# Optimization experiments

Hardware: AMD Instinct MI355X
Metric: run time of the kernel (lower is better)

Reference implementation:

```python
import jax, jax.numpy as jnp
import numpy as np

N = 16384      # nodes
E = 262144     # edges (avg degree 16)
R = 9          # relation types
D_IN = 384     # embed_size
D_H = 768      # hidden_size
N_CLASSES = 5


def setup_inputs() -> dict:
    key = jax.random.key(0)
    ks = jax.random.split(key, 11)
    s = 0.02
    return {
        "x": jax.random.normal(ks[0], (N, D_IN), jnp.float32),
        "edge_index": jax.random.randint(ks[1], (2, E), 0, N, dtype=jnp.int64)
        if jax.config.jax_enable_x64 else jax.random.randint(ks[1], (2, E), 0, N).astype(jnp.int32),
        "edge_type": jax.random.randint(ks[2], (E,), 0, R).astype(jnp.int32),
        "rel_W": jax.random.normal(ks[3], (R, D_H, D_IN), jnp.float32) * s,
        "rel_b": jax.random.normal(ks[4], (R, D_H), jnp.float32) * s,
        "norm_constants": jnp.ones((R,), jnp.float32),
        "mp_lin_W": jax.random.normal(ks[5], (D_H, D_H), jnp.float32) * s,
        "mp_lin_b": jax.random.normal(ks[6], (D_H,), jnp.float32) * s,
        "mp_self_W": jax.random.normal(ks[7], (D_H, D_H), jnp.float32) * s,
        "mp_self_b": jax.random.normal(ks[8], (D_H,), jnp.float32) * s,
        "out_W": jax.random.normal(ks[9], (N_CLASSES, D_H), jnp.float32) * s,
        "out_b": jax.random.normal(ks[10], (N_CLASSES,), jnp.float32) * s,
    }


def reference(x, edge_index, edge_type, rel_W, rel_b, norm_constants,
              mp_lin_W, mp_lin_b, mp_self_W, mp_self_b, out_W, out_b):
    n = x.shape[0]
    src = edge_index[0]  # j : message source (x_j)
    dst = edge_index[1]  # i : aggregation target

    # --- RelationAwareMP ---
    # edge_weights[i, j] from x @ x.T, computed per edge (identical math)
    ew = jnp.einsum('ed,ed->e', x[dst], x[src])                  # [E]
    norm = ew / norm_constants[edge_type]                        # [E]
    # per-relation linear applied to all nodes, then gathered per edge
    h = jnp.einsum('nd,rhd->rnh', x, rel_W) + rel_b[:, None, :]  # [R,N,H]
    msg = h[edge_type, src]                                      # [E,H]
    aggr = jax.ops.segment_sum(norm[:, None] * msg, dst, num_segments=n)
    x1 = jax.nn.relu(aggr)                                       # [N,H]

    # --- MP (add aggregation + self transform) ---
    self_x = x1 @ mp_self_W.T + mp_self_b
    hm = x1 @ mp_lin_W.T + mp_lin_b
    aggr2 = jax.ops.segment_sum(hm[src], dst, num_segments=n)
    x2 = jax.nn.relu(aggr2 + self_x)                             # [N,H]

    # --- readout ---
    pooled = x2.mean(axis=0)                                     # [H]
    return pooled @ out_W.T + out_b                              # [N_CLASSES]
```

## Files before the change

kernel.cpp:

```cpp
#include <hip/hip_runtime.h>

typedef unsigned char  u8;
typedef unsigned short u16;
typedef unsigned int   u32;

#define NN   16384
#define EE   262144
#define RR   9
#define DIN  384
#define DH   768
#define KSU  3456
#define KS   3488

typedef float  f32x4 __attribute__((ext_vector_type(4)));
typedef float  f32x2 __attribute__((ext_vector_type(2)));
typedef __bf16 b16x8 __attribute__((ext_vector_type(8)));

__device__ __forceinline__ u16 f2bf(float f){
  u32 u = __builtin_bit_cast(u32, f);
  u += 0x7fffu + ((u >> 16) & 1u);
  return (u16)(u >> 16);
}
__device__ __forceinline__ float bf2f(u16 h){
  u32 u = ((u32)h) << 16;
  return __builtin_bit_cast(float, u);
}
__device__ __forceinline__ float bflo(u32 u){ return __builtin_bit_cast(float, u << 16); }
__device__ __forceinline__ float bfhi(u32 u){ return __builtin_bit_cast(float, u & 0xffff0000u); }
__device__ __forceinline__ u32 pk2(float a, float b){
  return (u32)f2bf(a) | ((u32)f2bf(b) << 16);
}
__device__ __forceinline__ void gll16(const void* g, void* l){
  __builtin_amdgcn_global_load_lds((const __attribute__((address_space(1))) void*)g,
                                   (__attribute__((address_space(3))) void*)l, 16, 0, 0);
}

__global__ void k_count(const int* __restrict__ dst, int* __restrict__ counts){
  const int e = blockIdx.x*256 + threadIdx.x;
  if (e < EE) atomicAdd(&counts[dst[e]], 1);
}

__global__ __launch_bounds__(1024) void k_scan(const int* __restrict__ counts,
                                               int* __restrict__ starts,
                                               int* __restrict__ cursor){
  __shared__ int tot[1024];
  const int t = threadIdx.x;
  int loc[16]; int s = 0;
  #pragma unroll
  for (int j=0;j<16;j++){ loc[j] = counts[t*16+j]; s += loc[j]; }
  tot[t] = s;
  __syncthreads();
  for (int o=1;o<1024;o<<=1){
    int v = (t>=o) ? tot[t-o] : 0;
    __syncthreads();
    tot[t] += v;
    __syncthreads();
  }
  int run = tot[t] - s;
  #pragma unroll
  for (int j=0;j<16;j++){ starts[t*16+j] = run; cursor[t*16+j] = run; run += loc[j]; }
  if (t == 1023) starts[NN] = run;
}

__global__ void k_place(const int* __restrict__ src, const int* __restrict__ dst,
                        const int* __restrict__ et, int* __restrict__ cursor,
                        int* __restrict__ srcp, int* __restrict__ dstp,
                        int* __restrict__ rp){
  const int e = blockIdx.x*256 + threadIdx.x;
  if (e < EE){
    const int p = atomicAdd(&cursor[dst[e]], 1);
    srcp[p] = src[e];
    dstp[p] = dst[e];
    rp[p]   = et[e];
  }
}

#define NXP (NN*DIN/2)
#define NW1 (DH*KS)
#define NW2 (2*DH*DH)
__global__ __launch_bounds__(256) void k_conv(const float* __restrict__ x,
                                              const float* __restrict__ rW,
                                              const float* __restrict__ rb,
                                              const float* __restrict__ lW,
                                              const float* __restrict__ sW,
                                              u32* __restrict__ xb,
                                              u16* __restrict__ Wst,
                                              u16* __restrict__ WB){
  long j = (long)blockIdx.x*256 + threadIdx.x;
  if (j < NXP){
    const f32x2 v = ((const f32x2*)x)[j];
    xb[j] = pk2(v.x, v.y);
    return;
  }
  j -= NXP;
  if (j < NW1){
    const int hh = (int)(j / KS);
    const int k  = (int)(j - (long)hh*KS);
    float v;
    if (k < KSU){ const int r = k / DIN; const int d = k - r*DIN;
                  v = rW[((long)r*DH + hh)*DIN + d]; }
    else if (k < KSU + RR){ const int r = k - KSU; v = rb[(long)r*DH + hh]; }
    else v = 0.f;
    Wst[(long)hh*KS + k] = f2bf(v);
    return;
  }
  j -= NW1;
  const float v = (j < DH*DH) ? lW[j] : sW[j - DH*DH];
  WB[j] = f2bf(v);
}

__global__ __launch_bounds__(256, 4) void k_dots(const u32* __restrict__ xb,
                                                 const int* __restrict__ srcp,
                                                 const int* __restrict__ dstp,
                                                 const int* __restrict__ rp,
                                                 const float* __restrict__ nc,
                                                 float* __restrict__ normp){
  const int p = blockIdx.x*4 + (threadIdx.x >> 6);
  const int l = threadIdx.x & 63;
  const u32* xs = xb + (long)srcp[p]*192;
  const u32* xd = xb + (long)dstp[p]*192;
  float s = 0.f;
  #pragma unroll
  for (int j=0;j<3;j++){
    const u32 a = xs[l + 64*j], b = xd[l + 64*j];
    s += bflo(a)*bflo(b) + bfhi(a)*bfhi(b);
  }
  #pragma unroll
  for (int o=32;o;o>>=1) s += __shfl_xor(s, o);
  if (l == 0) normp[p] = s / nc[rp[p]];
}

__global__ __launch_bounds__(256, 3) void k_phase1f(const u32* __restrict__ xb,
                                                    const int* __restrict__ srcp,
                                                    const int* __restrict__ rp,
                                                    const float* __restrict__ normp,
                                                    const int* __restrict__ starts,
                                                    u16* __restrict__ s){
  const int w = threadIdx.x >> 6, l = threadIdx.x & 63;
  const int i = blockIdx.x*4 + w;
  float acc[RR][6];
  float cacc[RR];
  #pragma unroll
  for (int r=0;r<RR;r++){
    cacc[r] = 0.f;
    #pragma unroll
    for (int j=0;j<6;j++) acc[r][j] = 0.f;
  }
  const int e0 = starts[i], np = starts[i+1] - e0;

  u32 A0=0,A1=0,A2=0,B0=0,B1=0,B2=0,C0=0,C1=0,C2=0;
  float nA=0.f,nB=0.f,nC=0.f; int Ar=0,Br=0,Cr=0;

  #define LOADSLOT(S0,S1,S2,NR,RV,idx) { \
    const u32* xs_ = xb + (long)srcp[idx]*192; \
    S0 = xs_[l]; S1 = xs_[64+l]; S2 = xs_[128+l]; \
    NR = normp[idx]; RV = rp[idx]; }
  #define CONSUME(S0,S1,S2,NR,RV) { \
    const float f0=bflo(S0), f1=bfhi(S0), f2=bflo(S1), \
                f3=bfhi(S1), f4=bflo(S2), f5=bfhi(S2); \
    const float nm = NR; \
    switch (RV){ \
      case 0: cacc[0]+=nm; acc[0][0]+=nm*f0; acc[0][1]+=nm*f1; acc[0][2]+=nm*f2; acc[0][3]+=nm*f3; acc[0][4]+=nm*f4; acc[0][5]+=nm*f5; break; \
      case 1: cacc[1]+=nm; acc[1][0]+=nm*f0; acc[1][1]+=nm*f1; acc[1][2]+=nm*f2; acc[1][3]+=nm*f3; acc[1][4]+=nm*f4; acc[1][5]+=nm*f5; break; \
      case 2: cacc[2]+=nm; acc[2][0]+=nm*f0; acc[2][1]+=nm*f1; acc[2][2]+=nm*f2; acc[2][3]+=nm*f3; acc[2][4]+=nm*f4; acc[2][5]+=nm*f5; break; \
      case 3: cacc[3]+=nm; acc[3][0]+=nm*f0; acc[3][1]+=nm*f1; acc[3][2]+=nm*f2; acc[3][3]+=nm*f3; acc[3][4]+=nm*f4; acc[3][5]+=nm*f5; break; \
      case 4: cacc[4]+=nm; acc[4][0]+=nm*f0; acc[4][1]+=nm*f1; acc[4][2]+=nm*f2; acc[4][3]+=nm*f3; acc[4][4]+=nm*f4; acc[4][5]+=nm*f5; break; \
      case 5: cacc[5]+=nm; acc[5][0]+=nm*f0; acc[5][1]+=nm*f1; acc[5][2]+=nm*f2; acc[5][3]+=nm*f3; acc[5][4]+=nm*f4; acc[5][5]+=nm*f5; break; \
      case 6: cacc[6]+=nm; acc[6][0]+=nm*f0; acc[6][1]+=nm*f1; acc[6][2]+=nm*f2; acc[6][3]+=nm*f3; acc[6][4]+=nm*f4; acc[6][5]+=nm*f5; break; \
      case 7: cacc[7]+=nm; acc[7][0]+=nm*f0; acc[7][1]+=nm*f1; acc[7][2]+=nm*f2; acc[7][3]+=nm*f3; acc[7][4]+=nm*f4; acc[7][5]+=nm*f5; break; \
      default:cacc[8]+=nm; acc[8][0]+=nm*f0; acc[8][1]+=nm*f1; acc[8][2]+=nm*f2; acc[8][3]+=nm*f3; acc[8][4]+=nm*f4; acc[8][5]+=nm*f5; break; \
    } }

  if (np > 0) LOADSLOT(A0,A1,A2,nA,Ar,e0)
  if (np > 1) LOADSLOT(B0,B1,B2,nB,Br,e0+1)
  if (np > 2) LOADSLOT(C0,C1,C2,nC,Cr,e0+2)

  for (int p=0; p<np; p+=3){
    CONSUME(A0,A1,A2,nA,Ar)
    if (p+3 < np) LOADSLOT(A0,A1,A2,nA,Ar,e0+p+3)
    if (p+1 < np){
      CONSUME(B0,B1,B2,nB,Br)
      if (p+4 < np) LOADSLOT(B0,B1,B2,nB,Br,e0+p+4)
    }
    if (p+2 < np){
      CONSUME(C0,C1,C2,nC,Cr)
      if (p+5 < np) LOADSLOT(C0,C1,C2,nC,Cr,e0+p+5)
    }
  }
  #undef CONSUME
  #undef LOADSLOT

  u16* srow = s + (long)i*KS;
  #pragma unroll
  for (int r=0;r<RR;r++){
    #pragma unroll
    for (int seg=0;seg<3;seg++)
      ((u32*)(srow + r*DIN + seg*128))[l] = pk2(acc[r][seg*2], acc[r][seg*2+1]);
  }
  float cv = 0.f;
  #pragma unroll
  for (int r=0;r<RR;r++) cv = (l == r) ? cacc[r] : cv;
  if (l < 32) srow[KSU + l] = f2bf(l < RR ? cv : 0.f);
}

template<int MODE>
__global__ __launch_bounds__(256, 2)
void k_gemm_bt(const u16* __restrict__ A, const u16* __restrict__ B,
               int M, int N, int K,
               u16* __restrict__ O0, u16* __restrict__ O1,
               const float* __restrict__ b0, const float* __restrict__ b1)
{
  __shared__ __align__(16) u16 As[128*32];
  __shared__ __align__(16) u16 Bs[128*32];
  const int t  = threadIdx.x;
  const int wv = t >> 6;
  const int ln = t & 63;
  const int wm = wv >> 1, wn = wv & 1;
  const long m0 = (long)blockIdx.x * 128;
  const long n0 = (long)blockIdx.y * 128;

  const int ri    = ln >> 2;
  const int kw    = (ri + (ri >> 2)) & 3;
  const int skcol = (((ln & 3) - kw) & 3) * 8;

  f32x4 acc[4][4];
  #pragma unroll
  for (int i=0;i<4;i++)
    #pragma unroll
    for (int j=0;j<4;j++) acc[i][j] = {0.f,0.f,0.f,0.f};

  const int fr = ln & 15, fq = ln >> 4;
  const int kr    = (fr + (fr >> 2)) & 3;
  const int rdoff = ((fq + kr) & 3) * 8;
  const int nk = K >> 5;
  for (int kb=0; kb<nk; ++kb){
    const long k0 = (long)kb * 32;
    #pragma unroll
    for (int q=0;q<2;q++){
      const int seg = wv*2 + q;
      const int row = seg*16 + ri;
      gll16(A + (m0 + row)*(long)K + k0 + skcol, &As[seg*512]);
      gll16(B + (n0 + row)*(long)K + k0 + skcol, &Bs[seg*512]);
    }
    __syncthreads();
    b16x8 av[4], bv[4];
    #pragma unroll
    for (int i=0;i<4;i++){
      av[i] = *(const b16x8*)&As[(wm*64 + i*16 + fr)*32 + rdoff];
      bv[i] = *(const b16x8*)&Bs[(wn*64 + i*16 + fr)*32 + rdoff];
    }
    #pragma unroll
    for (int i=0;i<4;i++)
      #pragma unroll
      for (int j=0;j<4;j++)
        acc[i][j] = __builtin_amdgcn_mfma_f32_16x16x32_bf16(av[i], bv[j], acc[i][j], 0, 0, 0);
    __syncthreads();
  }

  #pragma unroll
  for (int i=0;i<4;i++){
    #pragma unroll
    for (int j=0;j<4;j++){
      #pragma unroll
      for (int r=0;r<4;r++){
        const long m = m0 + wm*64 + i*16 + fq*4 + r;
        const long n = n0 + wn*64 + j*16 + fr;
        float v = acc[i][j][r];
        if (MODE == 0){
          v = v > 0.f ? v : 0.f;
          O0[m*DH + n] = f2bf(v);
        } else {
          if (n < DH) O0[m*DH + n]      = f2bf(v + b0[n]);
          else        O1[m*DH + (n-DH)] = f2bf(v + b1[n-DH]);
        }
      }
    }
  }
}

__global__ __launch_bounds__(256, 4) void k_phase2(const u32* __restrict__ hm32,
                                                   const u32* __restrict__ sfx32,
                                                   const int* __restrict__ srcp,
                                                   const int* __restrict__ starts,
                                                   float* __restrict__ pooled8){
  const int w = threadIdx.x >> 6, l = threadIdx.x & 63;
  const int t = threadIdx.x;
  __shared__ float pl[DH];
  #pragma unroll
  for (int k=0;k<3;k++) pl[t + 256*k] = 0.f;
  __syncthreads();

  float po[12];
  #pragma unroll
  for (int j=0;j<12;j++) po[j] = 0.f;

  for (int q=0;q<2;q++){
    const int i = blockIdx.x*8 + w*2 + q;
    float a[12];
    #pragma unroll
    for (int j=0;j<12;j++) a[j] = 0.f;
    const int e0 = starts[i], np = starts[i+1] - e0;

    u32 A0=0,A1=0,A2=0,A3=0,A4=0,A5=0;
    u32 B0=0,B1=0,B2=0,B3=0,B4=0,B5=0;
    if (np > 0){
      const u32* hr = hm32 + (long)srcp[e0]*384;
      A0=hr[l]; A1=hr[64+l]; A2=hr[128+l]; A3=hr[192+l]; A4=hr[256+l]; A5=hr[320+l];
    }
    if (np > 1){
      const u32* hr = hm32 + (long)srcp[e0+1]*384;
      B0=hr[l]; B1=hr[64+l]; B2=hr[128+l]; B3=hr[192+l]; B4=hr[256+l]; B5=hr[320+l];
    }
    for (int p=0; p<np; p+=2){
      a[0]+=bflo(A0); a[1]+=bfhi(A0); a[2]+=bflo(A1); a[3] +=bfhi(A1);
      a[4]+=bflo(A2); a[5]+=bfhi(A2); a[6] +=bflo(A3); a[7] +=bfhi(A3);
      a[8]+=bflo(A4); a[9]+=bfhi(A4); a[10]+=bflo(A5); a[11]+=bfhi(A5);
      if (p+2 < np){
        const u32* hr = hm32 + (long)srcp[e0+p+2]*384;
        A0=hr[l]; A1=hr[64+l]; A2=hr[128+l]; A3=hr[192+l]; A4=hr[256+l]; A5=hr[320+l];
      }
      if (p+1 < np){
        a[0]+=bflo(B0); a[1]+=bfhi(B0); a[2] +=bflo(B1); a[3] +=bfhi(B1);
        a[4]+=bflo(B2); a[5]+=bfhi(B2); a[6] +=bflo(B3); a[7] +=bfhi(B3);
        a[8]+=bflo(B4); a[9]+=bfhi(B4); a[10]+=bflo(B5); a[11]+=bfhi(B5);
        if (p+3 < np){
          const u32* hr = hm32 + (long)srcp[e0+p+3]*384;
          B0=hr[l]; B1=hr[64+l]; B2=hr[128+l]; B3=hr[192+l]; B4=hr[256+l]; B5=hr[320+l];
        }
      }
    }
    const u32* sr = sfx32 + (long)i*384;
    #pragma unroll
    for (int j=0;j<6;j++){
      const u32 sv = sr[l + 64*j];
      float v0 = a[2*j]   + bflo(sv);
      float v1 = a[2*j+1] + bfhi(sv);
      po[2*j]   += v0 > 0.f ? v0 : 0.f;
      po[2*j+1] += v1 > 0.f ? v1 : 0.f;
    }
  }
  #pragma unroll
  for (int j=0;j<6;j++){
    atomicAdd(&pl[2*l   + 128*j], po[2*j]);
    atomicAdd(&pl[2*l+1 + 128*j], po[2*j+1]);
  }
  __syncthreads();
  float* pd = pooled8 + (blockIdx.x & 7)*DH;
  #pragma unroll
  for (int k=0;k<3;k++) atomicAdd(&pd[t + 256*k], pl[t + 256*k]);
}

__global__ __launch_bounds__(256) void k_final(const float* __restrict__ pooled8,
                                               const float* __restrict__ oW,
                                               const float* __restrict__ ob,
                                               float* __restrict__ out){
  __shared__ float ps[DH];
  __shared__ float red[256];
  const int t = threadIdx.x;
  for (int h=t; h<DH; h+=256){
    float s = 0.f;
    #pragma unroll
    for (int c=0;c<8;c++) s += pooled8[c*DH + h];
    ps[h] = s;
  }
  __syncthreads();
  for (int c=0;c<5;c++){
    float p = 0.f;
    for (int h=t; h<DH; h+=256) p += ps[h]*oW[c*DH + h];
    red[t] = p; __syncthreads();
    for (int o=128;o;o>>=1){ if (t<o) red[t]+=red[t+o]; __syncthreads(); }
    if (t == 0) out[c] = red[0]*(1.f/(float)NN) + ob[c];
    __syncthreads();
  }
}

extern "C" void kernel_launch(void* const* d_in, const int* in_sizes, int n_in,
                              void* d_out, int out_size, void* d_ws, size_t ws_size,
                              hipStream_t stream)
{
  (void)in_sizes; (void)n_in; (void)out_size; (void)ws_size;
  const float* x     = (const float*)d_in[0];
  const int*   ei    = (const int*)  d_in[1];
  const int*   et    = (const int*)  d_in[2];
  const float* relW  = (const float*)d_in[3];
  const float* relb  = (const float*)d_in[4];
  const float* nc    = (const float*)d_in[5];
  const float* linW  = (const float*)d_in[6];
  const float* linb  = (const float*)d_in[7];
  const float* selfW = (const float*)d_in[8];
  const float* selfb = (const float*)d_in[9];
  const float* outW  = (const float*)d_in[10];
  const float* outb  = (const float*)d_in[11];
  float* out = (float*)d_out;

  u8* w = (u8*)d_ws;
  int*   counts  = (int*)(w + 0);
  int*   starts  = (int*)(w + 65536);
  int*   cursor  = (int*)(w + 131328);
  int*   srcp    = (int*)(w + 196864);
  int*   dstp    = (int*)(w + 1245440);
  int*   rp      = (int*)(w + 2294016);
  float* normp   = (float*)(w + 3342592);
  u16*   Wst     = (u16*)(w + 4391168);
  u16*   WB      = (u16*)(w + 9748736);
  u16*   x1      = (u16*)(w + 12108032);
  u32*   xb      = (u32*)x1;
  float* pooled8 = (float*)(w + 37273856);
  u16*   S       = (u16*)(w + 37298432);
  u16*   hm      = S;
  u16*   sfx     = (u16*)(w + 37298432 + 25165824);

  const int* esrc = ei;
  const int* edst = ei + EE;

  hipMemsetAsync(counts, 0, NN*sizeof(int), stream);
  hipMemsetAsync(pooled8, 0, 8*DH*sizeof(float), stream);

  k_count <<<EE/256, 256, 0, stream>>>(edst, counts);
  k_scan  <<<1, 1024, 0, stream>>>(counts, starts, cursor);
  k_place <<<EE/256, 256, 0, stream>>>(esrc, edst, et, cursor, srcp, dstp, rp);
  k_conv  <<<(NXP + NW1 + NW2)/256, 256, 0, stream>>>(x, relW, relb, linW, selfW,
                                                      xb, Wst, WB);
  k_dots  <<<EE/4, 256, 0, stream>>>(xb, srcp, dstp, rp, nc, normp);
  k_phase1f<<<NN/4, 256, 0, stream>>>(xb, srcp, rp, normp, starts, S);
  k_gemm_bt<0><<<dim3(NN/128, DH/128), 256, 0, stream>>>(
      S, Wst, NN, DH, KS, x1, (u16*)nullptr, (const float*)nullptr, (const float*)nullptr);
  k_gemm_bt<1><<<dim3(NN/128, 2*DH/128), 256, 0, stream>>>(
      x1, WB, NN, 2*DH, DH, hm, sfx, linb, selfb);
  k_phase2<<<NN/8, 256, 0, stream>>>((const u32*)hm, (const u32*)sfx, srcp, starts, pooled8);
  k_final <<<1, 256, 0, stream>>>(pooled8, outW, outb, out);
}
```

Before: 542.7 us.

## Fuse edge dot products into aggregation, merge count into conversion, widen GEMM K-tile

Moves the per-edge x_dst·x_src dot product into the phase-1 aggregation kernel. The destination row is loaded once per warp and each message is reduced with wave shuffles, so the separate k_dots pass, the dstp/normp arrays and their traffic go away. Degree counting is folded into the conversion kernel, which removes one launch and one memset. The GEMM K-step grows from 32 to 64 with an XOR-swizzled LDS layout, and KS is padded to 3520 so it divides by 64. The cost is two shuffle reductions per edge pair inside the aggregation loop, a pipeline depth cut from 3 to 2, and larger shared-memory tiles.

```diff
diff --git a/kernel.cpp b/kernel.cpp
--- a/kernel.cpp
+++ b/kernel.cpp
@@ -10,7 +10,7 @@
 #define DIN  384
 #define DH   768
 #define KSU  3456
-#define KS   3488
+#define KS   3520
 
 typedef float  f32x4 __attribute__((ext_vector_type(4)));
 typedef float  f32x2 __attribute__((ext_vector_type(2)));
@@ -21,10 +21,6 @@
   u += 0x7fffu + ((u >> 16) & 1u);
   return (u16)(u >> 16);
 }
-__device__ __forceinline__ float bf2f(u16 h){
-  u32 u = ((u32)h) << 16;
-  return __builtin_bit_cast(float, u);
-}
 __device__ __forceinline__ float bflo(u32 u){ return __builtin_bit_cast(float, u << 16); }
 __device__ __forceinline__ float bfhi(u32 u){ return __builtin_bit_cast(float, u & 0xffff0000u); }
 __device__ __forceinline__ u32 pk2(float a, float b){
@@ -33,11 +29,6 @@
 __device__ __forceinline__ void gll16(const void* g, void* l){
   __builtin_amdgcn_global_load_lds((const __attribute__((address_space(1))) void*)g,
                                    (__attribute__((address_space(3))) void*)l, 16, 0, 0);
-}
-
-__global__ void k_count(const int* __restrict__ dst, int* __restrict__ counts){
-  const int e = blockIdx.x*256 + threadIdx.x;
-  if (e < EE) atomicAdd(&counts[dst[e]], 1);
 }
 
 __global__ __launch_bounds__(1024) void k_scan(const int* __restrict__ counts,
@@ -64,13 +55,11 @@
 
 __global__ void k_place(const int* __restrict__ src, const int* __restrict__ dst,
                         const int* __restrict__ et, int* __restrict__ cursor,
-                        int* __restrict__ srcp, int* __restrict__ dstp,
-                        int* __restrict__ rp){
+                        int* __restrict__ srcp, int* __restrict__ rp){
   const int e = blockIdx.x*256 + threadIdx.x;
   if (e < EE){
     const int p = atomicAdd(&cursor[dst[e]], 1);
     srcp[p] = src[e];
-    dstp[p] = dst[e];
     rp[p]   = et[e];
   }
 }
@@ -78,15 +67,19 @@
 #define NXP (NN*DIN/2)
 #define NW1 (DH*KS)
 #define NW2 (2*DH*DH)
-__global__ __launch_bounds__(256) void k_conv(const float* __restrict__ x,
+__global__ __launch_bounds__(256) void k_conv(const int* __restrict__ edst,
+                                              const float* __restrict__ x,
                                               const float* __restrict__ rW,
                                               const float* __restrict__ rb,
                                               const float* __restrict__ lW,
                                               const float* __restrict__ sW,
+                                              int* __restrict__ counts,
                                               u32* __restrict__ xb,
                                               u16* __restrict__ Wst,
                                               u16* __restrict__ WB){
   long j = (long)blockIdx.x*256 + threadIdx.x;
+  if (j < EE){ atomicAdd(&counts[edst[j]], 1); return; }
+  j -= EE;
   if (j < NXP){
     const f32x2 v = ((const f32x2*)x)[j];
     xb[j] = pk2(v.x, v.y);
@@ -109,35 +102,24 @@
   WB[j] = f2bf(v);
 }
 
-__global__ __launch_bounds__(256, 4) void k_dots(const u32* __restrict__ xb,
+__global__ __launch_bounds__(256) void k_phase1f(const u32* __restrict__ xb,
                                                  const int* __restrict__ srcp,
-                                                 const int* __restrict__ dstp,
                                                  const int* __restrict__ rp,
                                                  const float* __restrict__ nc,
-                                                 float* __restrict__ normp){
-  const int p = blockIdx.x*4 + (threadIdx.x >> 6);
-  const int l = threadIdx.x & 63;
-  const u32* xs = xb + (long)srcp[p]*192;
-  const u32* xd = xb + (long)dstp[p]*192;
-  float s = 0.f;
-  #pragma unroll
-  for (int j=0;j<3;j++){
-    const u32 a = xs[l + 64*j], b = xd[l + 64*j];
-    s += bflo(a)*bflo(b) + bfhi(a)*bfhi(b);
-  }
-  #pragma unroll
-  for (int o=32;o;o>>=1) s += __shfl_xor(s, o);
-  if (l == 0) normp[p] = s / nc[rp[p]];
-}
-
-__global__ __launch_bounds__(256, 3) void k_phase1f(const u32* __restrict__ xb,
-                                                    const int* __restrict__ srcp,
-                                                    const int* __restrict__ rp,
-                                                    const float* __restrict__ normp,
-                                                    const int* __restrict__ starts,
-                                                    u16* __restrict__ s){
+                                                 const int* __restrict__ starts,
+                                                 u16* __restrict__ s){
   const int w = threadIdx.x >> 6, l = threadIdx.x & 63;
   const int i = blockIdx.x*4 + w;
+  const u32* xr = xb + (long)i*192;
+  float xdf[6];
+  {
+    const u32 a = xr[l], b = xr[64+l], c = xr[128+l];
+    xdf[0]=bflo(a); xdf[1]=bfhi(a); xdf[2]=bflo(b);
+    xdf[3]=bfhi(b); xdf[4]=bflo(c); xdf[5]=bfhi(c);
+  }
+  float ncv[RR];
+  #pragma unroll
+  for (int r=0;r<RR;r++) ncv[r] = 1.0f / nc[r];
   float acc[RR][6];
   float cacc[RR];
   #pragma unroll
@@ -148,47 +130,57 @@
   }
   const int e0 = starts[i], np = starts[i+1] - e0;
 
-  u32 A0=0,A1=0,A2=0,B0=0,B1=0,B2=0,C0=0,C1=0,C2=0;
-  float nA=0.f,nB=0.f,nC=0.f; int Ar=0,Br=0,Cr=0;
-
-  #define LOADSLOT(S0,S1,S2,NR,RV,idx) { \
-    const u32* xs_ = xb + (long)srcp[idx]*192; \
-    S0 = xs_[l]; S1 = xs_[64+l]; S2 = xs_[128+l]; \
-    NR = normp[idx]; RV = rp[idx]; }
-  #define CONSUME(S0,S1,S2,NR,RV) { \
-    const float f0=bflo(S0), f1=bfhi(S0), f2=bflo(S1), \
-                f3=bfhi(S1), f4=bflo(S2), f5=bfhi(S2); \
-    const float nm = NR; \
-    switch (RV){ \
-      case 0: cacc[0]+=nm; acc[0][0]+=nm*f0; acc[0][1]+=nm*f1; acc[0][2]+=nm*f2; acc[0][3]+=nm*f3; acc[0][4]+=nm*f4; acc[0][5]+=nm*f5; break; \
-      case 1: cacc[1]+=nm; acc[1][0]+=nm*f0; acc[1][1]+=nm*f1; acc[1][2]+=nm*f2; acc[1][3]+=nm*f3; acc[1][4]+=nm*f4; acc[1][5]+=nm*f5; break; \
-      case 2: cacc[2]+=nm; acc[2][0]+=nm*f0; acc[2][1]+=nm*f1; acc[2][2]+=nm*f2; acc[2][3]+=nm*f3; acc[2][4]+=nm*f4; acc[2][5]+=nm*f5; break; \
-      case 3: cacc[3]+=nm; acc[3][0]+=nm*f0; acc[3][1]+=nm*f1; acc[3][2]+=nm*f2; acc[3][3]+=nm*f3; acc[3][4]+=nm*f4; acc[3][5]+=nm*f5; break; \
-      case 4: cacc[4]+=nm; acc[4][0]+=nm*f0; acc[4][1]+=nm*f1; acc[4][2]+=nm*f2; acc[4][3]+=nm*f3; acc[4][4]+=nm*f4; acc[4][5]+=nm*f5; break; \
-      case 5: cacc[5]+=nm; acc[5][0]+=nm*f0; acc[5][1]+=nm*f1; acc[5][2]+=nm*f2; acc[5][3]+=nm*f3; acc[5][4]+=nm*f4; acc[5][5]+=nm*f5; break; \
-      case 6: cacc[6]+=nm; acc[6][0]+=nm*f0; acc[6][1]+=nm*f1; acc[6][2]+=nm*f2; acc[6][3]+=nm*f3; acc[6][4]+=nm*f4; acc[6][5]+=nm*f5; break; \
-      case 7: cacc[7]+=nm; acc[7][0]+=nm*f0; acc[7][1]+=nm*f1; acc[7][2]+=nm*f2; acc[7][3]+=nm*f3; acc[7][4]+=nm*f4; acc[7][5]+=nm*f5; break; \
-      default:cacc[8]+=nm; acc[8][0]+=nm*f0; acc[8][1]+=nm*f1; acc[8][2]+=nm*f2; acc[8][3]+=nm*f3; acc[8][4]+=nm*f4; acc[8][5]+=nm*f5; break; \
-    } }
-
-  if (np > 0) LOADSLOT(A0,A1,A2,nA,Ar,e0)
-  if (np > 1) LOADSLOT(B0,B1,B2,nB,Br,e0+1)
-  if (np > 2) LOADSLOT(C0,C1,C2,nC,Cr,e0+2)
-
-  for (int p=0; p<np; p+=3){
-    CONSUME(A0,A1,A2,nA,Ar)
-    if (p+3 < np) LOADSLOT(A0,A1,A2,nA,Ar,e0+p+3)
-    if (p+1 < np){
-      CONSUME(B0,B1,B2,nB,Br)
-      if (p+4 < np) LOADSLOT(B0,B1,B2,nB,Br,e0+p+4)
-    }
+  u32 A0=0,A1=0,A2=0,B0=0,B1=0,B2=0; int Ar=0, Br=0;
+  if (np > 0){
+    const u32* xs = xb + (long)srcp[e0]*192;
+    A0=xs[l]; A1=xs[64+l]; A2=xs[128+l]; Ar=rp[e0];
+  }
+  if (np > 1){
+    const u32* xs = xb + (long)srcp[e0+1]*192;
+    B0=xs[l]; B1=xs[64+l]; B2=xs[128+l]; Br=rp[e0+1];
+  }
+
+  #define AXPY(R,CF,P) { const float nm_=(P)*ncv[R]; cacc[R]+=nm_; \
+    acc[R][0]+=nm_*CF[0]; acc[R][1]+=nm_*CF[1]; acc[R][2]+=nm_*CF[2]; \
+    acc[R][3]+=nm_*CF[3]; acc[R][4]+=nm_*CF[4]; acc[R][5]+=nm_*CF[5]; }
+  #define SW(CF,P,RV) switch (RV){ \
+      case 0: AXPY(0,CF,P) break; case 1: AXPY(1,CF,P) break; \
+      case 2: AXPY(2,CF,P) break; case 3: AXPY(3,CF,P) break; \
+      case 4: AXPY(4,CF,P) break; case 5: AXPY(5,CF,P) break; \
+      case 6: AXPY(6,CF,P) break; case 7: AXPY(7,CF,P) break; \
+      default: AXPY(8,CF,P) break; }
+
+  for (int p=0; p<np; p+=2){
+    const bool h2 = (p+1 < np);
+    const u32 a0=A0, a1=A1, a2=A2; const int ra=Ar;
+    const u32 b0=B0, b1=B1, b2=B2; const int rb=Br;
     if (p+2 < np){
-      CONSUME(C0,C1,C2,nC,Cr)
-      if (p+5 < np) LOADSLOT(C0,C1,C2,nC,Cr,e0+p+5)
-    }
-  }
-  #undef CONSUME
-  #undef LOADSLOT
+      const u32* xs = xb + (long)srcp[e0+p+2]*192;
+      A0=xs[l]; A1=xs[64+l]; A2=xs[128+l]; Ar=rp[e0+p+2];
+    }
+    if (p+3 < np){
+      const u32* xs = xb + (long)srcp[e0+p+3]*192;
+      B0=xs[l]; B1=xs[64+l]; B2=xs[128+l]; Br=rp[e0+p+3];
+    }
+    float fa[6], fb[6];
+    fa[0]=bflo(a0); fa[1]=bfhi(a0); fa[2]=bflo(a1);
+    fa[3]=bfhi(a1); fa[4]=bflo(a2); fa[5]=bfhi(a2);
+    fb[0]=bflo(b0); fb[1]=bfhi(b0); fb[2]=bflo(b1);
+    fb[3]=bfhi(b1); fb[4]=bflo(b2); fb[5]=bfhi(b2);
+    float pa = xdf[0]*fa[0] + xdf[1]*fa[1] + xdf[2]*fa[2]
+             + xdf[3]*fa[3] + xdf[4]*fa[4] + xdf[5]*fa[5];
+    float pb = xdf[0]*fb[0] + xdf[1]*fb[1] + xdf[2]*fb[2]
+             + xdf[3]*fb[3] + xdf[4]*fb[4] + xdf[5]*fb[5];
+    #pragma unroll
+    for (int o=32;o;o>>=1){
+      pa += __shfl_xor(pa, o);
+      pb += __shfl_xor(pb, o);
+    }
+    SW(fa,pa,ra)
+    if (h2){ SW(fb,pb,rb) }
+  }
+  #undef SW
+  #undef AXPY
 
   u16* srow = s + (long)i*KS;
   #pragma unroll
@@ -197,10 +189,13 @@
     for (int seg=0;seg<3;seg++)
       ((u32*)(srow + r*DIN + seg*128))[l] = pk2(acc[r][seg*2], acc[r][seg*2+1]);
   }
-  float cv = 0.f;
-  #pragma unroll
-  for (int r=0;r<RR;r++) cv = (l == r) ? cacc[r] : cv;
-  if (l < 32) srow[KSU + l] = f2bf(l < RR ? cv : 0.f);
+  float cv0 = 0.f, cv1 = 0.f;
+  #pragma unroll
+  for (int r=0;r<RR;r++){
+    cv0 = (2*l   == r) ? cacc[r] : cv0;
+    cv1 = (2*l+1 == r) ? cacc[r] : cv1;
+  }
+  if (l < 32) ((u32*)(srow + KSU))[l] = pk2(cv0, cv1);
 }
 
 template<int MODE>
@@ -210,8 +205,8 @@
                u16* __restrict__ O0, u16* __restrict__ O1,
                const float* __restrict__ b0, const float* __restrict__ b1)
 {
-  __shared__ __align__(16) u16 As[128*32];
-  __shared__ __align__(16) u16 Bs[128*32];
+  __shared__ __align__(16) u16 As[128*64];
+  __shared__ __align__(16) u16 Bs[128*64];
   const int t  = threadIdx.x;
   const int wv = t >> 6;
   const int ln = t & 63;
@@ -219,9 +214,8 @@
   const long m0 = (long)blockIdx.x * 128;
   const long n0 = (long)blockIdx.y * 128;
 
-  const int ri    = ln >> 2;
-  const int kw    = (ri + (ri >> 2)) & 3;
-  const int skcol = (((ln & 3) - kw) & 3) * 8;
+  const int srl = ln >> 3;
+  const int scc = ((ln & 7) ^ srl) * 8;
 
   f32x4 acc[4][4];
   #pragma unroll
@@ -230,30 +224,37 @@
     for (int j=0;j<4;j++) acc[i][j] = {0.f,0.f,0.f,0.f};
 
   const int fr = ln & 15, fq = ln >> 4;
-  const int kr    = (fr + (fr >> 2)) & 3;
-  const int rdoff = ((fq + kr) & 3) * 8;
-  const int nk = K >> 5;
+  const int nk = K >> 6;
   for (int kb=0; kb<nk; ++kb){
-    const long k0 = (long)kb * 32;
-    #pragma unroll
-    for (int q=0;q<2;q++){
-      const int seg = wv*2 + q;
-      const int row = seg*16 + ri;
-      gll16(A + (m0 + row)*(long)K + k0 + skcol, &As[seg*512]);
-      gll16(B + (n0 + row)*(long)K + k0 + skcol, &Bs[seg*512]);
+    const long k0 = (long)kb * 64;
+    #pragma unroll
+    for (int q=0;q<4;q++){
+      const int rbase = wv*32 + q*8;
+      const int row   = rbase + srl;
+      gll16(A + (m0 + row)*(long)K + k0 + scc, &As[rbase*64]);
+      gll16(B + (n0 + row)*(long)K + k0 + scc, &Bs[rbase*64]);
     }
     __syncthreads();
-    b16x8 av[4], bv[4];
+    b16x8 av0[4], bv0[4], av1[4], bv1[4];
     #pragma unroll
     for (int i=0;i<4;i++){
-      av[i] = *(const b16x8*)&As[(wm*64 + i*16 + fr)*32 + rdoff];
-      bv[i] = *(const b16x8*)&Bs[(wn*64 + i*16 + fr)*32 + rdoff];
+      const int pc0 = ((0*4 + fq) ^ (fr & 7))*8;
+      const int pc1 = ((1*4 + fq) ^ (fr & 7))*8;
+      av0[i] = *(const b16x8*)&As[(wm*64 + i*16 + fr)*64 + pc0];
+      bv0[i] = *(const b16x8*)&Bs[(wn*64 + i*16 + fr)*64 + pc0];
+      av1[i] = *(const b16x8*)&As[(wm*64 + i*16 + fr)*64 + pc1];
+      bv1[i] = *(const b16x8*)&Bs[(wn*64 + i*16 + fr)*64 + pc1];
     }
     #pragma unroll
     for (int i=0;i<4;i++)
       #pragma unroll
       for (int j=0;j<4;j++)
-        acc[i][j] = __builtin_amdgcn_mfma_f32_16x16x32_bf16(av[i], bv[j], acc[i][j], 0, 0, 0);
+        acc[i][j] = __builtin_amdgcn_mfma_f32_16x16x32_bf16(av0[i], bv0[j], acc[i][j], 0, 0, 0);
+    #pragma unroll
+    for (int i=0;i<4;i++)
+      #pragma unroll
+      for (int j=0;j<4;j++)
+        acc[i][j] = __builtin_amdgcn_mfma_f32_16x16x32_bf16(av1[i], bv1[j], acc[i][j], 0, 0, 0);
     __syncthreads();
   }
 
@@ -395,34 +396,29 @@
 
   u8* w = (u8*)d_ws;
   int*   counts  = (int*)(w + 0);
-  int*   starts  = (int*)(w + 65536);
-  int*   cursor  = (int*)(w + 131328);
-  int*   srcp    = (int*)(w + 196864);
-  int*   dstp    = (int*)(w + 1245440);
-  int*   rp      = (int*)(w + 2294016);
-  float* normp   = (float*)(w + 3342592);
-  u16*   Wst     = (u16*)(w + 4391168);
-  u16*   WB      = (u16*)(w + 9748736);
-  u16*   x1      = (u16*)(w + 12108032);
+  float* pooled8 = (float*)(w + 65536);
+  int*   starts  = (int*)(w + 90112);
+  int*   cursor  = (int*)(w + 155904);
+  int*   srcp    = (int*)(w + 221440);
+  int*   rp      = (int*)(w + 1270016);
+  u16*   Wst     = (u16*)(w + 2318592);
+  u16*   WB      = (u16*)(w + 7725312);
+  u16*   x1      = (u16*)(w + 10084608);
   u32*   xb      = (u32*)x1;
-  float* pooled8 = (float*)(w + 37273856);
-  u16*   S       = (u16*)(w + 37298432);
+  u16*   S       = (u16*)(w + 35250432);
   u16*   hm      = S;
-  u16*   sfx     = (u16*)(w + 37298432 + 25165824);
+  u16*   sfx     = (u16*)(w + 35250432 + 25165824);
 
   const int* esrc = ei;
   const int* edst = ei + EE;
 
-  hipMemsetAsync(counts, 0, NN*sizeof(int), stream);
-  hipMemsetAsync(pooled8, 0, 8*DH*sizeof(float), stream);
-
-  k_count <<<EE/256, 256, 0, stream>>>(edst, counts);
+  hipMemsetAsync(w, 0, 90112, stream);
+
+  k_conv  <<<(EE + NXP + NW1 + NW2)/256, 256, 0, stream>>>(
+      edst, x, relW, relb, linW, selfW, counts, xb, Wst, WB);
   k_scan  <<<1, 1024, 0, stream>>>(counts, starts, cursor);
-  k_place <<<EE/256, 256, 0, stream>>>(esrc, edst, et, cursor, srcp, dstp, rp);
-  k_conv  <<<(NXP + NW1 + NW2)/256, 256, 0, stream>>>(x, relW, relb, linW, selfW,
-                                                      xb, Wst, WB);
-  k_dots  <<<EE/4, 256, 0, stream>>>(xb, srcp, dstp, rp, nc, normp);
-  k_phase1f<<<NN/4, 256, 0, stream>>>(xb, srcp, rp, normp, starts, S);
+  k_place <<<EE/256, 256, 0, stream>>>(esrc, edst, et, cursor, srcp, rp);
+  k_phase1f<<<NN/4, 256, 0, stream>>>(xb, srcp, rp, nc, starts, S);
   k_gemm_bt<0><<<dim3(NN/128, DH/128), 256, 0, stream>>>(
       S, Wst, NN, DH, KS, x1, (u16*)nullptr, (const float*)nullptr, (const float*)nullptr);
   k_gemm_bt<1><<<dim3(NN/128, 2*DH/128), 256, 0, stream>>>(
```

New measurement: 650.2 us. 19.8% more time.
